# Optimization experiments

Measured on AMD Instinct MI355X. Metric: run time of the kernel, lower is better.

## Reference

```python
import jax, jax.numpy as jnp
import numpy as np

B, N_BOX, NUM_CLASSES = 32, 50, 20
FEATURE_SIZES = np.array([[52, 52], [26, 26], [13, 13]])
NUM_CENG = FEATURE_SIZES[:, 0] * FEATURE_SIZES[:, 1]            # [2704, 676, 169]
NUM_TOTAL = int((NUM_CENG * 3).sum())                            # 10647
ANCS_SCALE = np.array([[10, 13], [16, 30], [33, 23], [30, 61], [62, 45],
                       [59, 119], [116, 90], [156, 198], [373, 326]], dtype=np.float32) / 416.0
NEG_IOU_THRESHOLD = 0.5
NUM_NEG = 1000
EPS = 1e-7

def _build_anchor_grid():
    # rows ordered: level(52,26,13) -> cell (row-major) -> 3 anchors per cell
    out = []
    for lvl in range(3):
        f = int(FEATURE_SIZES[lvl, 0])
        ys, xs = np.meshgrid(np.arange(f), np.arange(f), indexing='ij')
        xy = (np.stack([xs, ys], -1).reshape(-1, 2).astype(np.float32)) / f  # cell corner (col/f,row/f)
        xy3 = np.repeat(xy, 3, axis=0)                                       # [f*f*3, 2]
        wh3 = np.tile(ANCS_SCALE[lvl * 3:(lvl + 1) * 3], (f * f, 1))
        out.append(np.concatenate([xy3, wh3], 1))
    return np.concatenate(out, 0)                                            # [10647, 4]

ANCS = jnp.asarray(_build_anchor_grid())
FSIZES = jnp.asarray(np.repeat(FEATURE_SIZES[:, 0].astype(np.float32), NUM_CENG * 3))  # [10647]
OFF_CENG = jnp.asarray([0.0, 2704.0, 3380.0])   # prefix sums of NUM_CENG
FW_LVL = jnp.asarray([52.0, 26.0, 13.0])


def _xywh2ltrb(xywh):
    return jnp.concatenate([xywh[..., :2] - xywh[..., 2:] * 0.5,
                            xywh[..., :2] + xywh[..., 2:] * 0.5], -1)


def _ciou(a, b):
    # a, b: broadcastable [..., 4] ltrb -> CIoU [...]
    lt = jnp.maximum(a[..., :2], b[..., :2])
    rb = jnp.minimum(a[..., 2:], b[..., 2:])
    wh = jnp.clip(rb - lt, 0.0)
    inter = wh[..., 0] * wh[..., 1]
    wa = a[..., 2] - a[..., 0]; ha = a[..., 3] - a[..., 1]
    wb = b[..., 2] - b[..., 0]; hb = b[..., 3] - b[..., 1]
    union = wa * ha + wb * hb - inter
    iou = inter / (union + EPS)
    clt = jnp.minimum(a[..., :2], b[..., :2])
    crb = jnp.maximum(a[..., 2:], b[..., 2:])
    cwh = crb - clt
    c2 = cwh[..., 0] ** 2 + cwh[..., 1] ** 2 + EPS
    ctr_a = (a[..., :2] + a[..., 2:]) * 0.5
    ctr_b = (b[..., :2] + b[..., 2:]) * 0.5
    rho2 = jnp.sum((ctr_a - ctr_b) ** 2, -1)
    v = (4.0 / (jnp.pi ** 2)) * (jnp.arctan(wa / (ha + EPS)) - jnp.arctan(wb / (hb + EPS))) ** 2
    alpha = jax.lax.stop_gradient(v / (1.0 - iou + v + EPS))
    return iou - rho2 / c2 - alpha * v


def _bce(p, t):
    p = jnp.clip(p, EPS, 1.0 - EPS)
    return -(t * jnp.log(p) + (1.0 - t) * jnp.log(1.0 - p))


def _per_image(p, boxes, labels):
    # p: [10647, 25], boxes: [N,4] ltrb, labels: [N] (1-based)
    N = boxes.shape[0]
    bxy = (boxes[:, :2] + boxes[:, 2:]) * 0.5
    bwh = boxes[:, 2:] - boxes[:, :2]
    # ---- anchor-target matching (source's loop always takes argmax anchor) ----
    p1xy = jnp.repeat(bxy, 9, axis=0)                                       # [N*9, 2]
    fpairs = jnp.repeat(jnp.asarray(FEATURE_SIZES, jnp.float32), 3, axis=0)  # [9, 2]
    p2f = jnp.tile(fpairs, (N, 1))                                          # [N*9, 2]
    colrow = jnp.floor(p1xy * p2f)                                          # (col, row) per box/anchor
    anc_xy = colrow / p2f
    anc_wh = jnp.tile(jnp.asarray(ANCS_SCALE), (N, 1))
    anc_ltrb = _xywh2ltrb(jnp.concatenate([anc_xy, anc_wh], 1))
    ids = jnp.arange(N, dtype=boxes.dtype)
    iou_m = _ciou(boxes[:, None, :] + ids[:, None, None],
                  anc_ltrb[None, :, :] + jnp.repeat(ids, 9)[None, :, None])  # [N, N*9]
    k = jnp.argmax(iou_m, axis=1) % 9                                       # best anchor id 0..8
    lvl = k // 3                                                            # (source quirk: //len(NUMS_ANC))
    cr = colrow[jnp.arange(N) * 9 + k]                                      # [N, 2]
    off_cr = cr[:, 1] * FW_LVL[lvl] + cr[:, 0]
    midx = ((OFF_CENG[lvl] + off_cr) * 3.0 + lvl.astype(jnp.float32)).astype(jnp.int32)  # [N]
    # ---- decode predictions ----
    p_box_xy = p[:, :2] / FSIZES[:, None] + ANCS[:, :2]
    p_box_wh = jnp.exp(p[:, 2:4]) * ANCS[:, 2:]
    p_ltrb = _xywh2ltrb(jnp.concatenate([p_box_xy, p_box_wh], -1))          # [10647, 4]
    # ---- positive losses ----
    pcls = p[midx, 5:]                                                      # [N, C]
    t = jax.nn.one_hot(labels - 1, NUM_CLASSES, dtype=pcls.dtype)
    l_cls = _bce(pcls, t).sum()
    pconf = p[midx, 4]
    l_conf_p = (-jnp.log(jnp.clip(pconf, EPS, 1.0 - EPS))).sum()
    ciou_pos = _ciou(boxes, p_ltrb[midx])                                   # [N]
    w = 2.0 - bwh[:, 0] * bwh[:, 1]
    l_box = (w * (1.0 - ciou_pos)).sum()
    # ---- negative conf loss (replicates filtered-coordinate indexing) ----
    iou_all = _ciou(boxes[:, None, :], p_ltrb[None, :, :])                  # [N, 10647]
    mx = iou_all.max(axis=0)
    mask = mx < NEG_IOU_THRESHOLD
    key = jnp.where(mask, mx, jnp.inf)
    order = jnp.argsort(key)                                                # masked-in first, ascending
    rank = jnp.cumsum(mask) - 1                                             # filtered coordinate per row
    neg_idx = rank[order][:NUM_NEG]                                         # == source's _max_index[:NUM_NEG]
    pneg = p[neg_idx, 4]
    l_conf_n = (-jnp.log(jnp.clip(1.0 - pneg, EPS, 1.0 - EPS))).sum()
    nf = jnp.asarray(N, p.dtype)
    return l_cls / nf, l_box / nf, l_conf_p / nf, l_conf_n


def setup_inputs() -> dict:
    key = jax.random.key(0)
    k1, k2, k3, k4 = jax.random.split(key, 4)
    p_yolo_ts = jax.random.uniform(k1, (B, NUM_TOTAL, 4 + 1 + NUM_CLASSES),
                                   dtype=jnp.float32, minval=1e-4, maxval=1.0 - 1e-4)
    cxy = jax.random.uniform(k2, (B, N_BOX, 2), minval=0.15, maxval=0.85)
    wh = jax.random.uniform(k3, (B, N_BOX, 2), minval=0.05, maxval=0.25)
    boxes = jnp.concatenate([cxy - wh * 0.5, cxy + wh * 0.5], -1).astype(jnp.float32)
    labels = jax.random.randint(k4, (B, N_BOX), 1, NUM_CLASSES + 1, dtype=jnp.int32)
    return {"p_yolo_ts": p_yolo_ts, "boxes": boxes, "labels": labels}


def reference(p_yolo_ts, boxes, labels):
    l_cls, l_box, l_cp, l_cn = jax.vmap(_per_image)(p_yolo_ts, boxes, labels)
    return l_cp.mean() + l_cn.mean() + l_box.mean() + l_cls.mean()
```

## Files before the change

### kernel.cpp

```cpp
#include <hip/hip_runtime.h>

namespace {

constexpr int BB   = 32;
constexpr int NBOX = 50;
constexpr int NCLS = 20;
constexpr int NT   = 10647;
constexpr int NNEG = 1000;
constexpr float EPS = 1e-7f;
constexpr float PI4 = (float)(4.0 / 9.869604401089358);

__device__ __constant__ float c_aw[9] = {10.f/416.f,16.f/416.f,33.f/416.f,30.f/416.f,62.f/416.f,59.f/416.f,116.f/416.f,156.f/416.f,373.f/416.f};
__device__ __constant__ float c_ah[9] = {13.f/416.f,30.f/416.f,23.f/416.f,61.f/416.f,45.f/416.f,119.f/416.f,90.f/416.f,198.f/416.f,326.f/416.f};

__device__ __forceinline__ float fastrcp(float x) {
  return __builtin_amdgcn_rcpf(x);
}

__device__ __forceinline__ float dciou(float al, float at, float ar, float ab,
                                       float bl, float bt, float br, float bb,
                                       float atanA, float atanB) {
  float ltx = fmaxf(al, bl), lty = fmaxf(at, bt);
  float rbx = fminf(ar, br), rby = fminf(ab, bb);
  float wx = fmaxf(rbx - ltx, 0.f), wy = fmaxf(rby - lty, 0.f);
  float inter = wx * wy;
  float wa = ar - al, ha = ab - at;
  float wb = br - bl, hb = bb - bt;
  float uni = wa * ha + wb * hb - inter;
  float iou = inter / (uni + EPS);
  float cw = fmaxf(ar, br) - fminf(al, bl);
  float ch = fmaxf(ab, bb) - fminf(at, bt);
  float c2 = cw * cw + ch * ch + EPS;
  float dx = (al + ar) * 0.5f - (bl + br) * 0.5f;
  float dy = (at + ab) * 0.5f - (bt + bb) * 0.5f;
  float rho2 = dx * dx + dy * dy;
  float dat = atanA - atanB;
  float v = PI4 * (dat * dat);
  float alpha = v / (1.f - iou + v + EPS);
  return iou - rho2 / c2 - alpha * v;
}

__device__ __forceinline__ float dciou_h(float4 A, float4 E,
                                         float bl, float bt, float br, float bb,
                                         float areaB,
                                         float cxb, float cyb, float atanB) {
  float ltx = fmaxf(A.x, bl), lty = fmaxf(A.y, bt);
  float rbx = fminf(A.z, br), rby = fminf(A.w, bb);
  float wx = fmaxf(rbx - ltx, 0.f), wy = fmaxf(rby - lty, 0.f);
  float inter = wx * wy;
  float uni = E.w + areaB - inter;
  float iou = inter * fastrcp(uni + EPS);
  float cw = fmaxf(A.z, br) - fminf(A.x, bl);
  float ch = fmaxf(A.w, bb) - fminf(A.y, bt);
  float c2 = cw * cw + ch * ch + EPS;
  float dx = E.x - cxb;
  float dy = E.y - cyb;
  float rho2 = dx * dx + dy * dy;
  float dat = E.z - atanB;
  float v = PI4 * (dat * dat);
  float alpha = v * fastrcp(1.f - iou + v + EPS);
  return iou - rho2 * fastrcp(c2) - alpha * v;
}

__device__ __forceinline__ int wave_incl_scan(int x, int lane) {
  #pragma unroll
  for (int off = 1; off < 64; off <<= 1) {
    int y = __shfl_up(x, off);
    if (lane >= off) x += y;
  }
  return x;
}

__global__ __launch_bounds__(256) void k_decode_mx(const float* __restrict__ p,
                            const float* __restrict__ boxes,
                            unsigned long long* __restrict__ comp) {
  const int b = blockIdx.y;
  const int tid = threadIdx.x;
  const int par = tid & 1;
  const int j = blockIdx.x * 128 + (tid >> 1);

  __shared__ float4 sA[NBOX];
  __shared__ float4 sE[NBOX];
  if (tid < NBOX) {
    const float* bp = boxes + (b * NBOX + tid) * 4;
    float l = bp[0], t = bp[1], r = bp[2], d = bp[3];
    sA[tid] = make_float4(l, t, r, d);
    float wa = r - l, ha = d - t;
    float cx = (l + r) * 0.5f, cy = (t + d) * 0.5f;
    sE[tid] = make_float4(cx, cy, atanf(wa / (ha + EPS)), wa * ha);
  }
  __syncthreads();
  if (j >= NT) return;

  int lvl, jb0, f;
  if (j < 8112)       { lvl = 0; jb0 = 0;     f = 52; }
  else if (j < 10140) { lvl = 1; jb0 = 8112;  f = 26; }
  else                { lvl = 2; jb0 = 10140; f = 13; }
  int jj = j - jb0;
  int cell = jj / 3, a = jj % 3 + lvl * 3;
  int x = cell % f, y = cell / f;
  float ff = (float)f;
  const float* pr = p + ((size_t)b * NT + j) * 25;
  float px = pr[0] / ff + (float)x / ff;
  float py = pr[1] / ff + (float)y / ff;
  float pw = expf(pr[2]) * c_aw[a];
  float ph = expf(pr[3]) * c_ah[a];
  float bl = px - pw * 0.5f, bt = py - ph * 0.5f;
  float br = px + pw * 0.5f, bbv = py + ph * 0.5f;
  float wb = br - bl, hb = bbv - bt;
  float areab = wb * hb;
  float cxb = (bl + br) * 0.5f, cyb = (bt + bbv) * 0.5f;
  float atb = atanf(wb / (hb + EPS));

  float mx = -INFINITY;
  #pragma unroll 5
  for (int i = par; i < NBOX; i += 2) {
    float v = dciou_h(sA[i], sE[i], bl, bt, br, bbv, areab, cxb, cyb, atb);
    mx = fmaxf(mx, v);
  }
  mx = fmaxf(mx, __shfl_xor(mx, 1));

  if (par == 0) {
    float key = (mx < 0.5f) ? mx : INFINITY;
    unsigned int u = __float_as_uint(key);
    u = (u & 0x80000000u) ? ~u : (u | 0x80000000u);
    comp[(size_t)b * NT + j] = ((unsigned long long)u << 14) | (unsigned long long)j;
  }
}

__global__ __launch_bounds__(1024) void k_neg2(const unsigned long long* __restrict__ comp,
                                               const float* __restrict__ p,
                                               float* __restrict__ lcn) {
  int b = blockIdx.x;
  const unsigned long long* c = comp + (size_t)b * NT;
  const int tid = threadIdx.x, lane = tid & 63, wave = tid >> 6;

  __shared__ int hist[4096];
  __shared__ int s_w[16];
  __shared__ unsigned long long s_pref;
  __shared__ int s_rem;
  __shared__ int s_digit;
  __shared__ int s_rem_next;
  __shared__ int s_cnt;
  __shared__ float s_facc[16];
  __shared__ int s_tot[11][16];
  __shared__ int s_off[11][16];

  unsigned long long v[11];
  #pragma unroll
  for (int k = 0; k < 11; ++k) {
    int j = k * 1024 + tid;
    v[k] = (j < NT) ? c[j] : ~0ull;
  }

  int wincl[11];
  #pragma unroll
  for (int k = 0; k < 11; ++k) {
    unsigned long long x = v[k];
    int flag = ((x >> 14) < 0xFF800000ull) ? 1 : 0;
    int incl = wave_incl_scan(flag, lane);
    wincl[k] = incl;
    if (lane == 63) s_tot[k][wave] = incl;
  }
  __syncthreads();
  if (wave == 0) {
    int i0 = lane * 3;
    int a0 = (i0     < 176) ? s_tot[i0 / 16][i0 % 16] : 0;
    int a1 = (i0 + 1 < 176) ? s_tot[(i0 + 1) / 16][(i0 + 1) % 16] : 0;
    int a2 = (i0 + 2 < 176) ? s_tot[(i0 + 2) / 16][(i0 + 2) % 16] : 0;
    int lsum = a0 + a1 + a2;
    int linc = wave_incl_scan(lsum, lane);
    int lexc = linc - lsum;
    if (i0     < 176) s_off[i0 / 16][i0 % 16] = lexc;
    if (i0 + 1 < 176) s_off[(i0 + 1) / 16][(i0 + 1) % 16] = lexc + a0;
    if (i0 + 2 < 176) s_off[(i0 + 2) / 16][(i0 + 2) % 16] = lexc + a0 + a1;
    if (lane == 63) s_cnt = linc;
  }
  if (tid == 0) { s_pref = 0ull; s_rem = NNEG - 1; }
  __syncthreads();
  const bool spec = (s_cnt >= NNEG);

  for (int pass = 0; pass < 4; ++pass) {
    int lo = 36 - pass * 12;
    for (int h = tid; h < 4096; h += 1024) hist[h] = 0;
    __syncthreads();
    unsigned long long pref = s_pref;
    #pragma unroll
    for (int k = 0; k < 11; ++k) {
      unsigned long long x = v[k];
      bool fin = ((x >> 14) < 0xFF800000ull);
      if ((!spec || fin) && (x >> (lo + 12)) == (pref >> (lo + 12)))
        atomicAdd(&hist[(int)((x >> lo) & 4095ull)], 1);
    }
    __syncthreads();
    int base = tid * 4;
    int c0 = hist[base], c1 = hist[base + 1], c2 = hist[base + 2], c3 = hist[base + 3];
    int tsum = c0 + c1 + c2 + c3;
    int incl = wave_incl_scan(tsum, lane);
    if (lane == 63) s_w[wave] = incl;
    __syncthreads();
    if (wave == 0) {
      int wv = (lane < 16) ? s_w[lane] : 0;
      int wincl2 = wave_incl_scan(wv, lane);
      if (lane < 16) s_w[lane] = wincl2 - wv;
    }
    __syncthreads();
    int excl = incl - tsum + s_w[wave];
    int rem = s_rem;
    int p0 = excl, p1 = p0 + c0, p2 = p1 + c1, p3 = p2 + c2;
    if (rem >= p0 && rem < p0 + c0) { s_digit = base + 0; s_rem_next = rem - p0; }
    if (rem >= p1 && rem < p1 + c1) { s_digit = base + 1; s_rem_next = rem - p1; }
    if (rem >= p2 && rem < p2 + c2) { s_digit = base + 2; s_rem_next = rem - p2; }
    if (rem >= p3 && rem < p3 + c3) { s_digit = base + 3; s_rem_next = rem - p3; }
    __syncthreads();
    if (tid == 0) {
      s_pref |= ((unsigned long long)s_digit) << lo;
      s_rem = s_rem_next;
    }
    __syncthreads();
  }
  const unsigned long long T = s_pref;

  float acc = 0.f;
  const float* pb = p + (size_t)b * NT * 25;
  #pragma unroll
  for (int k = 0; k < 11; ++k) {
    unsigned long long x = v[k];
    if (x <= T) {
      int idx = s_off[k][wave] + wincl[k] - 1;
      if (idx < 0) idx += NT;
      float q = 1.f - pb[(size_t)idx * 25 + 4];
      q = fminf(fmaxf(q, EPS), 1.f - EPS);
      acc += -logf(q);
    }
  }

  #pragma unroll
  for (int off = 32; off > 0; off >>= 1) acc += __shfl_down(acc, off);
  if (lane == 0) s_facc[wave] = acc;
  __syncthreads();
  if (tid == 0) {
    float s = 0.f;
    #pragma unroll
    for (int w = 0; w < 16; ++w) s += s_facc[w];
    lcn[b] = s;
  }
}

__global__ __launch_bounds__(64) void k_pos(const float* __restrict__ p, const float* __restrict__ boxes,
                      const int* __restrict__ labels,
                      float* __restrict__ pcls, float* __restrict__ pbox, float* __restrict__ pcp) {
  const int i = blockIdx.x;
  const int b = blockIdx.y;
  const int lane = threadIdx.x;

  __shared__ float scx[NBOX], scy[NBOX];
  if (lane < NBOX) {
    const float* bp = boxes + (b * NBOX + lane) * 4;
    float l = bp[0], t = bp[1], r = bp[2], d = bp[3];
    scx[lane] = (l + r) * 0.5f;
    scy[lane] = (t + d) * 0.5f;
  }
  __syncthreads();

  const float* bi = boxes + (b * NBOX + i) * 4;
  float bl0 = bi[0], bt0 = bi[1], br0 = bi[2], bd0 = bi[3];
  float fi = (float)i;
  float al = bl0 + fi, at = bt0 + fi, ar = br0 + fi, ad = bd0 + fi;
  float wa = ar - al, ha = ad - at;
  float atanA = atanf(wa / (ha + EPS));

  float bestv = -INFINITY; int bestm = 1 << 30;
  #pragma unroll
  for (int m = lane; m < 9 * NBOX; m += 64) {
    int jb = m / 9, a = m % 9;
    float fa = (a < 3) ? 52.f : (a < 6 ? 26.f : 13.f);
    float col = floorf(scx[jb] * fa);
    float row = floorf(scy[jb] * fa);
    float ax = col / fa, ay = row / fa;
    float aw = c_aw[a], ah = c_ah[a];
    float fj = (float)jb;
    float bl = (ax - aw * 0.5f) + fj;
    float bt = (ay - ah * 0.5f) + fj;
    float br = (ax + aw * 0.5f) + fj;
    float bd = (ay + ah * 0.5f) + fj;
    float wb = br - bl, hb = bd - bt;
    float atanB = atanf(wb / (hb + EPS));
    float v = dciou(al, at, ar, ad, bl, bt, br, bd, atanA, atanB);
    if (v > bestv) { bestv = v; bestm = m; }
  }
  #pragma unroll
  for (int off = 32; off > 0; off >>= 1) {
    float ov = __shfl_down(bestv, off);
    int om = __shfl_down(bestm, off);
    if (ov > bestv || (ov == bestv && om < bestm)) { bestv = ov; bestm = om; }
  }
  int bm = __shfl(bestm, 0);

  int k = bm % 9;
  int lvl = k / 3;
  float fk = (k < 3) ? 52.f : (k < 6 ? 26.f : 13.f);
  float col = floorf(scx[i] * fk);
  float row = floorf(scy[i] * fk);
  float offc = (lvl == 0) ? 0.f : (lvl == 1 ? 2704.f : 3380.f);
  int midx = (int)((offc + row * fk + col) * 3.0f + (float)lvl);

  const float* pr = p + ((size_t)b * NT + midx) * 25;
  int lab = labels[b * NBOX + i] - 1;

  float lc = 0.f;
  if (lane < NCLS) {
    float pc = pr[5 + lane];
    pc = fminf(fmaxf(pc, EPS), 1.f - EPS);
    float tt = (lane == lab) ? 1.f : 0.f;
    lc = -(tt * logf(pc) + (1.f - tt) * logf(1.f - pc));
  }
  #pragma unroll
  for (int off = 32; off > 0; off >>= 1) lc += __shfl_down(lc, off);

  if (lane == 0) {
    pcls[b * NBOX + i] = lc;
    float pc4 = pr[4];
    pc4 = fminf(fmaxf(pc4, EPS), 1.f - EPS);
    pcp[b * NBOX + i] = -logf(pc4);

    int lvl2, jb0, f2;
    if (midx < 8112)       { lvl2 = 0; jb0 = 0;     f2 = 52; }
    else if (midx < 10140) { lvl2 = 1; jb0 = 8112;  f2 = 26; }
    else                   { lvl2 = 2; jb0 = 10140; f2 = 13; }
    int jj2 = midx - jb0;
    int cell2 = jj2 / 3, a2 = jj2 % 3 + lvl2 * 3;
    int xx = cell2 % f2, yy = cell2 / f2;
    float ff2 = (float)f2;
    float px = pr[0] / ff2 + (float)xx / ff2;
    float py = pr[1] / ff2 + (float)yy / ff2;
    float pw = expf(pr[2]) * c_aw[a2];
    float ph = expf(pr[3]) * c_ah[a2];
    float pbl = px - pw * 0.5f, pbt = py - ph * 0.5f;
    float pbr = px + pw * 0.5f, pbd = py + ph * 0.5f;

    float wb = pbr - pbl, hb = pbd - pbt;
    float atanB = atanf(wb / (hb + EPS));
    float wa0 = br0 - bl0, ha0 = bd0 - bt0;
    float atanA0 = atanf(wa0 / (ha0 + EPS));
    float cp = dciou(bl0, bt0, br0, bd0, pbl, pbt, pbr, pbd, atanA0, atanB);
    float w = 2.f - wa0 * ha0;
    pbox[b * NBOX + i] = w * (1.f - cp);
  }
}

__global__ void k_final(const float* __restrict__ pcls, const float* __restrict__ pbox,
                        const float* __restrict__ pcp, const float* __restrict__ lcn,
                        float* __restrict__ out) {
  int lane = threadIdx.x;
  float s = 0.f;
  if (lane < BB) {
    float a = 0.f, bx = 0.f, cp = 0.f;
    for (int i = 0; i < NBOX; ++i) {
      a  += pcls[lane * NBOX + i];
      bx += pbox[lane * NBOX + i];
      cp += pcp[lane * NBOX + i];
    }
    s = (a + bx + cp) / (float)NBOX + lcn[lane];
  }
  #pragma unroll
  for (int off = 32; off > 0; off >>= 1) s += __shfl_down(s, off);
  if (lane == 0) out[0] = s / (float)BB;
}

}

extern "C" void kernel_launch(void* const* d_in, const int* in_sizes, int n_in,
                              void* d_out, int out_size, void* d_ws, size_t ws_size,
                              hipStream_t stream) {
  const float* p      = (const float*)d_in[0];
  const float* boxes  = (const float*)d_in[1];
  const int*   labels = (const int*)d_in[2];
  float* out = (float*)d_out;

  char* ws = (char*)d_ws;
  size_t off = 0;
  unsigned long long* comp = (unsigned long long*)(ws + off); off += (size_t)BB * NT * sizeof(unsigned long long);
  float* pcls = (float*)(ws + off);                off += BB * NBOX * sizeof(float);
  float* pbox = (float*)(ws + off);                off += BB * NBOX * sizeof(float);
  float* pcp  = (float*)(ws + off);                off += BB * NBOX * sizeof(float);
  float* lcn  = (float*)(ws + off);                off += BB * sizeof(float);

  dim3 g1((NT + 127) / 128, BB);
  k_decode_mx<<<g1, 256, 0, stream>>>(p, boxes, comp);
  k_neg2<<<BB, 1024, 0, stream>>>(comp, p, lcn);
  k_pos<<<dim3(NBOX, BB), 64, 0, stream>>>(p, boxes, labels, pcls, pbox, pcp);
  k_final<<<1, 64, 0, stream>>>(pcls, pbox, pcp, lcn, out);
}
```

Baseline: 60.43 us.

## Precompute GT box features in prep kernel and use one thread per anchor

Adds a small k_prep kernel that writes the 8 derived floats per ground-truth box (ltrb, center, atan of aspect, area) to workspace. The decode kernel then reads them as uniform 32-byte vector loads from global memory instead of staging them in shared memory behind a barrier. It also switches from two threads per anchor plus a shuffle to one thread per anchor over all 50 boxes, with index clamping instead of an early return. This removes the per-block atan prologue and the syncthreads, at the cost of an extra kernel launch, half as many blocks and longer serial loops per thread.

```diff
diff --git a/kernel.cpp b/kernel.cpp
--- a/kernel.cpp
+++ b/kernel.cpp
@@ -9,6 +9,8 @@
 constexpr int NNEG = 1000;
 constexpr float EPS = 1e-7f;
 constexpr float PI4 = (float)(4.0 / 9.869604401089358);
+
+typedef __attribute__((ext_vector_type(8))) float f32x8;
 
 __device__ __constant__ float c_aw[9] = {10.f/416.f,16.f/416.f,33.f/416.f,30.f/416.f,62.f/416.f,59.f/416.f,116.f/416.f,156.f/416.f,373.f/416.f};
 __device__ __constant__ float c_ah[9] = {13.f/416.f,30.f/416.f,23.f/416.f,61.f/416.f,45.f/416.f,119.f/416.f,90.f/416.f,198.f/416.f,326.f/416.f};
@@ -40,23 +42,23 @@
   return iou - rho2 / c2 - alpha * v;
 }
 
-__device__ __forceinline__ float dciou_h(float4 A, float4 E,
+__device__ __forceinline__ float dciou_e(f32x8 e,
                                          float bl, float bt, float br, float bb,
                                          float areaB,
                                          float cxb, float cyb, float atanB) {
-  float ltx = fmaxf(A.x, bl), lty = fmaxf(A.y, bt);
-  float rbx = fminf(A.z, br), rby = fminf(A.w, bb);
+  float ltx = fmaxf(e[0], bl), lty = fmaxf(e[1], bt);
+  float rbx = fminf(e[2], br), rby = fminf(e[3], bb);
   float wx = fmaxf(rbx - ltx, 0.f), wy = fmaxf(rby - lty, 0.f);
   float inter = wx * wy;
-  float uni = E.w + areaB - inter;
+  float uni = e[7] + areaB - inter;
   float iou = inter * fastrcp(uni + EPS);
-  float cw = fmaxf(A.z, br) - fminf(A.x, bl);
-  float ch = fmaxf(A.w, bb) - fminf(A.y, bt);
+  float cw = fmaxf(e[2], br) - fminf(e[0], bl);
+  float ch = fmaxf(e[3], bb) - fminf(e[1], bt);
   float c2 = cw * cw + ch * ch + EPS;
-  float dx = E.x - cxb;
-  float dy = E.y - cyb;
+  float dx = e[4] - cxb;
+  float dy = e[5] - cyb;
   float rho2 = dx * dx + dy * dy;
-  float dat = E.z - atanB;
+  float dat = e[6] - atanB;
   float v = PI4 * (dat * dat);
   float alpha = v * fastrcp(1.f - iou + v + EPS);
   return iou - rho2 * fastrcp(c2) - alpha * v;
@@ -71,36 +73,36 @@
   return x;
 }
 
+__global__ __launch_bounds__(64) void k_prep(const float* __restrict__ boxes,
+                                             float* __restrict__ e8) {
+  int b = blockIdx.x, t = threadIdx.x;
+  if (t >= NBOX) return;
+  const float* bp = boxes + (b * NBOX + t) * 4;
+  float l = bp[0], tt = bp[1], r = bp[2], d = bp[3];
+  float wa = r - l, ha = d - tt;
+  float* o = e8 + (b * NBOX + t) * 8;
+  o[0] = l; o[1] = tt; o[2] = r; o[3] = d;
+  o[4] = (l + r) * 0.5f;
+  o[5] = (tt + d) * 0.5f;
+  o[6] = atanf(wa / (ha + EPS));
+  o[7] = wa * ha;
+}
+
 __global__ __launch_bounds__(256) void k_decode_mx(const float* __restrict__ p,
-                            const float* __restrict__ boxes,
+                            const float* __restrict__ e8,
                             unsigned long long* __restrict__ comp) {
   const int b = blockIdx.y;
-  const int tid = threadIdx.x;
-  const int par = tid & 1;
-  const int j = blockIdx.x * 128 + (tid >> 1);
-
-  __shared__ float4 sA[NBOX];
-  __shared__ float4 sE[NBOX];
-  if (tid < NBOX) {
-    const float* bp = boxes + (b * NBOX + tid) * 4;
-    float l = bp[0], t = bp[1], r = bp[2], d = bp[3];
-    sA[tid] = make_float4(l, t, r, d);
-    float wa = r - l, ha = d - t;
-    float cx = (l + r) * 0.5f, cy = (t + d) * 0.5f;
-    sE[tid] = make_float4(cx, cy, atanf(wa / (ha + EPS)), wa * ha);
-  }
-  __syncthreads();
-  if (j >= NT) return;
-
-  int lvl, jb0, f;
-  if (j < 8112)       { lvl = 0; jb0 = 0;     f = 52; }
-  else if (j < 10140) { lvl = 1; jb0 = 8112;  f = 26; }
-  else                { lvl = 2; jb0 = 10140; f = 13; }
-  int jj = j - jb0;
+  const int j = blockIdx.x * 256 + threadIdx.x;
+  const int jc = (j < NT) ? j : (NT - 1);
+
+  int lvl = (jc < 8112) ? 0 : ((jc < 10140) ? 1 : 2);
+  int jb0 = (lvl == 0) ? 0 : ((lvl == 1) ? 8112 : 10140);
+  int f   = (lvl == 0) ? 52 : ((lvl == 1) ? 26 : 13);
+  int jj = jc - jb0;
   int cell = jj / 3, a = jj % 3 + lvl * 3;
   int x = cell % f, y = cell / f;
   float ff = (float)f;
-  const float* pr = p + ((size_t)b * NT + j) * 25;
+  const float* pr = p + ((size_t)b * NT + jc) * 25;
   float px = pr[0] / ff + (float)x / ff;
   float py = pr[1] / ff + (float)y / ff;
   float pw = expf(pr[2]) * c_aw[a];
@@ -112,15 +114,15 @@
   float cxb = (bl + br) * 0.5f, cyb = (bt + bbv) * 0.5f;
   float atb = atanf(wb / (hb + EPS));
 
+  const f32x8* eb = (const f32x8*)(e8 + b * NBOX * 8);
   float mx = -INFINITY;
   #pragma unroll 5
-  for (int i = par; i < NBOX; i += 2) {
-    float v = dciou_h(sA[i], sE[i], bl, bt, br, bbv, areab, cxb, cyb, atb);
+  for (int i = 0; i < NBOX; ++i) {
+    float v = dciou_e(eb[i], bl, bt, br, bbv, areab, cxb, cyb, atb);
     mx = fmaxf(mx, v);
   }
-  mx = fmaxf(mx, __shfl_xor(mx, 1));
-
-  if (par == 0) {
+
+  if (j < NT) {
     float key = (mx < 0.5f) ? mx : INFINITY;
     unsigned int u = __float_as_uint(key);
     u = (u & 0x80000000u) ? ~u : (u | 0x80000000u);
@@ -381,13 +383,15 @@
   char* ws = (char*)d_ws;
   size_t off = 0;
   unsigned long long* comp = (unsigned long long*)(ws + off); off += (size_t)BB * NT * sizeof(unsigned long long);
+  float* e8   = (float*)(ws + off);                off += (size_t)BB * NBOX * 8 * sizeof(float);
   float* pcls = (float*)(ws + off);                off += BB * NBOX * sizeof(float);
   float* pbox = (float*)(ws + off);                off += BB * NBOX * sizeof(float);
   float* pcp  = (float*)(ws + off);                off += BB * NBOX * sizeof(float);
   float* lcn  = (float*)(ws + off);                off += BB * sizeof(float);
 
-  dim3 g1((NT + 127) / 128, BB);
-  k_decode_mx<<<g1, 256, 0, stream>>>(p, boxes, comp);
+  k_prep<<<BB, 64, 0, stream>>>(boxes, e8);
+  dim3 g1((NT + 255) / 256, BB);
+  k_decode_mx<<<g1, 256, 0, stream>>>(p, e8, comp);
   k_neg2<<<BB, 1024, 0, stream>>>(comp, p, lcn);
   k_pos<<<dim3(NBOX, BB), 64, 0, stream>>>(p, boxes, labels, pcls, pbox, pcp);
   k_final<<<1, 64, 0, stream>>>(pcls, pbox, pcp, lcn, out);
```

After: 69.29 us. 14.7% more time.

## Merge positive-match kernel into decode kernel and split box loop four ways

Applied to the files above, without the earlier changes.

Folds the per-GT positive-loss computation into the decode/max-IoU kernel as extra blocks along the grid's x dimension, removing one kernel launch. The decode path now uses 4 threads per prediction (64 predictions per block) instead of 2, doubling the number of blocks for more parallelism, and reduces across the 4 lanes with two xor shuffles. The positive path packs 4 GTs per 256-thread block, one per wave. This trades a launch for a heterogeneous kernel, and the extra shuffles and shorter per-thread loops may or may not pay off.

```diff
diff --git a/kernel.cpp b/kernel.cpp
--- a/kernel.cpp
+++ b/kernel.cpp
@@ -7,6 +7,8 @@
 constexpr int NCLS = 20;
 constexpr int NT   = 10647;
 constexpr int NNEG = 1000;
+constexpr int DEC_BLOCKS = (NT + 63) / 64;
+constexpr int POS_BLOCKS = (NBOX + 3) / 4;
 constexpr float EPS = 1e-7f;
 constexpr float PI4 = (float)(4.0 / 9.869604401089358);
 
@@ -71,60 +73,164 @@
   return x;
 }
 
-__global__ __launch_bounds__(256) void k_decode_mx(const float* __restrict__ p,
+__global__ __launch_bounds__(256) void k_main(const float* __restrict__ p,
                             const float* __restrict__ boxes,
-                            unsigned long long* __restrict__ comp) {
+                            const int* __restrict__ labels,
+                            unsigned long long* __restrict__ comp,
+                            float* __restrict__ pcls, float* __restrict__ pbox,
+                            float* __restrict__ pcp) {
   const int b = blockIdx.y;
   const int tid = threadIdx.x;
-  const int par = tid & 1;
-  const int j = blockIdx.x * 128 + (tid >> 1);
-
-  __shared__ float4 sA[NBOX];
-  __shared__ float4 sE[NBOX];
-  if (tid < NBOX) {
-    const float* bp = boxes + (b * NBOX + tid) * 4;
-    float l = bp[0], t = bp[1], r = bp[2], d = bp[3];
-    sA[tid] = make_float4(l, t, r, d);
-    float wa = r - l, ha = d - t;
-    float cx = (l + r) * 0.5f, cy = (t + d) * 0.5f;
-    sE[tid] = make_float4(cx, cy, atanf(wa / (ha + EPS)), wa * ha);
-  }
-  __syncthreads();
-  if (j >= NT) return;
-
-  int lvl, jb0, f;
-  if (j < 8112)       { lvl = 0; jb0 = 0;     f = 52; }
-  else if (j < 10140) { lvl = 1; jb0 = 8112;  f = 26; }
-  else                { lvl = 2; jb0 = 10140; f = 13; }
-  int jj = j - jb0;
-  int cell = jj / 3, a = jj % 3 + lvl * 3;
-  int x = cell % f, y = cell / f;
-  float ff = (float)f;
-  const float* pr = p + ((size_t)b * NT + j) * 25;
-  float px = pr[0] / ff + (float)x / ff;
-  float py = pr[1] / ff + (float)y / ff;
-  float pw = expf(pr[2]) * c_aw[a];
-  float ph = expf(pr[3]) * c_ah[a];
-  float bl = px - pw * 0.5f, bt = py - ph * 0.5f;
-  float br = px + pw * 0.5f, bbv = py + ph * 0.5f;
-  float wb = br - bl, hb = bbv - bt;
-  float areab = wb * hb;
-  float cxb = (bl + br) * 0.5f, cyb = (bt + bbv) * 0.5f;
-  float atb = atanf(wb / (hb + EPS));
-
-  float mx = -INFINITY;
-  #pragma unroll 5
-  for (int i = par; i < NBOX; i += 2) {
-    float v = dciou_h(sA[i], sE[i], bl, bt, br, bbv, areab, cxb, cyb, atb);
-    mx = fmaxf(mx, v);
-  }
-  mx = fmaxf(mx, __shfl_xor(mx, 1));
-
-  if (par == 0) {
-    float key = (mx < 0.5f) ? mx : INFINITY;
-    unsigned int u = __float_as_uint(key);
-    u = (u & 0x80000000u) ? ~u : (u | 0x80000000u);
-    comp[(size_t)b * NT + j] = ((unsigned long long)u << 14) | (unsigned long long)j;
+
+  if (blockIdx.x < DEC_BLOCKS) {
+    __shared__ float4 sA[NBOX];
+    __shared__ float4 sE[NBOX];
+    if (tid < NBOX) {
+      const float* bp = boxes + (b * NBOX + tid) * 4;
+      float l = bp[0], t = bp[1], r = bp[2], d = bp[3];
+      sA[tid] = make_float4(l, t, r, d);
+      float wa = r - l, ha = d - t;
+      sE[tid] = make_float4((l + r) * 0.5f, (t + d) * 0.5f,
+                            atanf(wa / (ha + EPS)), wa * ha);
+    }
+    __syncthreads();
+
+    const int q = tid & 3;
+    const int j = blockIdx.x * 64 + (tid >> 2);
+    if (j >= NT) return;
+
+    int lvl = (j < 8112) ? 0 : ((j < 10140) ? 1 : 2);
+    int jb0 = (lvl == 0) ? 0 : ((lvl == 1) ? 8112 : 10140);
+    int f   = (lvl == 0) ? 52 : ((lvl == 1) ? 26 : 13);
+    int jj = j - jb0;
+    int cell = jj / 3, a = jj % 3 + lvl * 3;
+    int x = cell % f, y = cell / f;
+    float ff = (float)f;
+    const float* pr = p + ((size_t)b * NT + j) * 25;
+    float px = pr[0] / ff + (float)x / ff;
+    float py = pr[1] / ff + (float)y / ff;
+    float pw = expf(pr[2]) * c_aw[a];
+    float ph = expf(pr[3]) * c_ah[a];
+    float bl = px - pw * 0.5f, bt = py - ph * 0.5f;
+    float br = px + pw * 0.5f, bbv = py + ph * 0.5f;
+    float wb = br - bl, hb = bbv - bt;
+    float areab = wb * hb;
+    float cxb = (bl + br) * 0.5f, cyb = (bt + bbv) * 0.5f;
+    float atb = atanf(wb / (hb + EPS));
+
+    float mx = -INFINITY;
+    #pragma unroll 4
+    for (int i = q; i < NBOX; i += 4) {
+      float v = dciou_h(sA[i], sE[i], bl, bt, br, bbv, areab, cxb, cyb, atb);
+      mx = fmaxf(mx, v);
+    }
+    mx = fmaxf(mx, __shfl_xor(mx, 1));
+    mx = fmaxf(mx, __shfl_xor(mx, 2));
+
+    if (q == 0) {
+      float key = (mx < 0.5f) ? mx : INFINITY;
+      unsigned int u = __float_as_uint(key);
+      u = (u & 0x80000000u) ? ~u : (u | 0x80000000u);
+      comp[(size_t)b * NT + j] = ((unsigned long long)u << 14) | (unsigned long long)j;
+    }
+  } else {
+    const int lane = tid & 63;
+    const int wave = tid >> 6;
+    const int i = (blockIdx.x - DEC_BLOCKS) * 4 + wave;
+
+    __shared__ float scx[NBOX], scy[NBOX];
+    if (tid < NBOX) {
+      const float* bp = boxes + (b * NBOX + tid) * 4;
+      float l = bp[0], t = bp[1], r = bp[2], d = bp[3];
+      scx[tid] = (l + r) * 0.5f;
+      scy[tid] = (t + d) * 0.5f;
+    }
+    __syncthreads();
+    if (i >= NBOX) return;
+
+    const float* bi = boxes + (b * NBOX + i) * 4;
+    float bl0 = bi[0], bt0 = bi[1], br0 = bi[2], bd0 = bi[3];
+    float fi = (float)i;
+    float al = bl0 + fi, at = bt0 + fi, ar = br0 + fi, ad = bd0 + fi;
+    float wa = ar - al, ha = ad - at;
+    float atanA = atanf(wa / (ha + EPS));
+
+    float bestv = -INFINITY; int bestm = 1 << 30;
+    #pragma unroll
+    for (int m = lane; m < 9 * NBOX; m += 64) {
+      int jb = m / 9, aa = m % 9;
+      float fa = (aa < 3) ? 52.f : (aa < 6 ? 26.f : 13.f);
+      float col = floorf(scx[jb] * fa);
+      float row = floorf(scy[jb] * fa);
+      float ax = col / fa, ay = row / fa;
+      float aw = c_aw[aa], ah = c_ah[aa];
+      float fj = (float)jb;
+      float bl = (ax - aw * 0.5f) + fj;
+      float bt = (ay - ah * 0.5f) + fj;
+      float br = (ax + aw * 0.5f) + fj;
+      float bd = (ay + ah * 0.5f) + fj;
+      float wb = br - bl, hb = bd - bt;
+      float atanB = atanf(wb / (hb + EPS));
+      float v = dciou(al, at, ar, ad, bl, bt, br, bd, atanA, atanB);
+      if (v > bestv) { bestv = v; bestm = m; }
+    }
+    #pragma unroll
+    for (int off = 32; off > 0; off >>= 1) {
+      float ov = __shfl_down(bestv, off);
+      int om = __shfl_down(bestm, off);
+      if (ov > bestv || (ov == bestv && om < bestm)) { bestv = ov; bestm = om; }
+    }
+    int bm = __shfl(bestm, 0);
+
+    int k = bm % 9;
+    int lvl = k / 3;
+    float fk = (k < 3) ? 52.f : (k < 6 ? 26.f : 13.f);
+    float col = floorf(scx[i] * fk);
+    float row = floorf(scy[i] * fk);
+    float offc = (lvl == 0) ? 0.f : (lvl == 1 ? 2704.f : 3380.f);
+    int midx = (int)((offc + row * fk + col) * 3.0f + (float)lvl);
+
+    const float* prm = p + ((size_t)b * NT + midx) * 25;
+    int lab = labels[b * NBOX + i] - 1;
+
+    float lc = 0.f;
+    if (lane < NCLS) {
+      float pc = prm[5 + lane];
+      pc = fminf(fmaxf(pc, EPS), 1.f - EPS);
+      float tt = (lane == lab) ? 1.f : 0.f;
+      lc = -(tt * logf(pc) + (1.f - tt) * logf(1.f - pc));
+    }
+    #pragma unroll
+    for (int off = 32; off > 0; off >>= 1) lc += __shfl_down(lc, off);
+
+    if (lane == 0) {
+      pcls[b * NBOX + i] = lc;
+      float pc4 = prm[4];
+      pc4 = fminf(fmaxf(pc4, EPS), 1.f - EPS);
+      pcp[b * NBOX + i] = -logf(pc4);
+
+      int lvl2 = (midx < 8112) ? 0 : ((midx < 10140) ? 1 : 2);
+      int jb0 = (lvl2 == 0) ? 0 : ((lvl2 == 1) ? 8112 : 10140);
+      int f2  = (lvl2 == 0) ? 52 : ((lvl2 == 1) ? 26 : 13);
+      int jj2 = midx - jb0;
+      int cell2 = jj2 / 3, a2 = jj2 % 3 + lvl2 * 3;
+      int xx = cell2 % f2, yy = cell2 / f2;
+      float ff2 = (float)f2;
+      float px = prm[0] / ff2 + (float)xx / ff2;
+      float py = prm[1] / ff2 + (float)yy / ff2;
+      float pw = expf(prm[2]) * c_aw[a2];
+      float ph = expf(prm[3]) * c_ah[a2];
+      float pbl = px - pw * 0.5f, pbt = py - ph * 0.5f;
+      float pbr = px + pw * 0.5f, pbd = py + ph * 0.5f;
+
+      float wb = pbr - pbl, hb = pbd - pbt;
+      float atanB = atanf(wb / (hb + EPS));
+      float wa0 = br0 - bl0, ha0 = bd0 - bt0;
+      float atanA0 = atanf(wa0 / (ha0 + EPS));
+      float cp = dciou(bl0, bt0, br0, bd0, pbl, pbt, pbr, pbd, atanA0, atanB);
+      float w = 2.f - wa0 * ha0;
+      pbox[b * NBOX + i] = w * (1.f - cp);
+    }
   }
 }
 
@@ -247,108 +353,6 @@
   }
 }
 
-__global__ __launch_bounds__(64) void k_pos(const float* __restrict__ p, const float* __restrict__ boxes,
-                      const int* __restrict__ labels,
-                      float* __restrict__ pcls, float* __restrict__ pbox, float* __restrict__ pcp) {
-  const int i = blockIdx.x;
-  const int b = blockIdx.y;
-  const int lane = threadIdx.x;
-
-  __shared__ float scx[NBOX], scy[NBOX];
-  if (lane < NBOX) {
-    const float* bp = boxes + (b * NBOX + lane) * 4;
-    float l = bp[0], t = bp[1], r = bp[2], d = bp[3];
-    scx[lane] = (l + r) * 0.5f;
-    scy[lane] = (t + d) * 0.5f;
-  }
-  __syncthreads();
-
-  const float* bi = boxes + (b * NBOX + i) * 4;
-  float bl0 = bi[0], bt0 = bi[1], br0 = bi[2], bd0 = bi[3];
-  float fi = (float)i;
-  float al = bl0 + fi, at = bt0 + fi, ar = br0 + fi, ad = bd0 + fi;
-  float wa = ar - al, ha = ad - at;
-  float atanA = atanf(wa / (ha + EPS));
-
-  float bestv = -INFINITY; int bestm = 1 << 30;
-  #pragma unroll
-  for (int m = lane; m < 9 * NBOX; m += 64) {
-    int jb = m / 9, a = m % 9;
-    float fa = (a < 3) ? 52.f : (a < 6 ? 26.f : 13.f);
-    float col = floorf(scx[jb] * fa);
-    float row = floorf(scy[jb] * fa);
-    float ax = col / fa, ay = row / fa;
-    float aw = c_aw[a], ah = c_ah[a];
-    float fj = (float)jb;
-    float bl = (ax - aw * 0.5f) + fj;
-    float bt = (ay - ah * 0.5f) + fj;
-    float br = (ax + aw * 0.5f) + fj;
-    float bd = (ay + ah * 0.5f) + fj;
-    float wb = br - bl, hb = bd - bt;
-    float atanB = atanf(wb / (hb + EPS));
-    float v = dciou(al, at, ar, ad, bl, bt, br, bd, atanA, atanB);
-    if (v > bestv) { bestv = v; bestm = m; }
-  }
-  #pragma unroll
-  for (int off = 32; off > 0; off >>= 1) {
-    float ov = __shfl_down(bestv, off);
-    int om = __shfl_down(bestm, off);
-    if (ov > bestv || (ov == bestv && om < bestm)) { bestv = ov; bestm = om; }
-  }
-  int bm = __shfl(bestm, 0);
-
-  int k = bm % 9;
-  int lvl = k / 3;
-  float fk = (k < 3) ? 52.f : (k < 6 ? 26.f : 13.f);
-  float col = floorf(scx[i] * fk);
-  float row = floorf(scy[i] * fk);
-  float offc = (lvl == 0) ? 0.f : (lvl == 1 ? 2704.f : 3380.f);
-  int midx = (int)((offc + row * fk + col) * 3.0f + (float)lvl);
-
-  const float* pr = p + ((size_t)b * NT + midx) * 25;
-  int lab = labels[b * NBOX + i] - 1;
-
-  float lc = 0.f;
-  if (lane < NCLS) {
-    float pc = pr[5 + lane];
-    pc = fminf(fmaxf(pc, EPS), 1.f - EPS);
-    float tt = (lane == lab) ? 1.f : 0.f;
-    lc = -(tt * logf(pc) + (1.f - tt) * logf(1.f - pc));
-  }
-  #pragma unroll
-  for (int off = 32; off > 0; off >>= 1) lc += __shfl_down(lc, off);
-
-  if (lane == 0) {
-    pcls[b * NBOX + i] = lc;
-    float pc4 = pr[4];
-    pc4 = fminf(fmaxf(pc4, EPS), 1.f - EPS);
-    pcp[b * NBOX + i] = -logf(pc4);
-
-    int lvl2, jb0, f2;
-    if (midx < 8112)       { lvl2 = 0; jb0 = 0;     f2 = 52; }
-    else if (midx < 10140) { lvl2 = 1; jb0 = 8112;  f2 = 26; }
-    else                   { lvl2 = 2; jb0 = 10140; f2 = 13; }
-    int jj2 = midx - jb0;
-    int cell2 = jj2 / 3, a2 = jj2 % 3 + lvl2 * 3;
-    int xx = cell2 % f2, yy = cell2 / f2;
-    float ff2 = (float)f2;
-    float px = pr[0] / ff2 + (float)xx / ff2;
-    float py = pr[1] / ff2 + (float)yy / ff2;
-    float pw = expf(pr[2]) * c_aw[a2];
-    float ph = expf(pr[3]) * c_ah[a2];
-    float pbl = px - pw * 0.5f, pbt = py - ph * 0.5f;
-    float pbr = px + pw * 0.5f, pbd = py + ph * 0.5f;
-
-    float wb = pbr - pbl, hb = pbd - pbt;
-    float atanB = atanf(wb / (hb + EPS));
-    float wa0 = br0 - bl0, ha0 = bd0 - bt0;
-    float atanA0 = atanf(wa0 / (ha0 + EPS));
-    float cp = dciou(bl0, bt0, br0, bd0, pbl, pbt, pbr, pbd, atanA0, atanB);
-    float w = 2.f - wa0 * ha0;
-    pbox[b * NBOX + i] = w * (1.f - cp);
-  }
-}
-
 __global__ void k_final(const float* __restrict__ pcls, const float* __restrict__ pbox,
                         const float* __restrict__ pcp, const float* __restrict__ lcn,
                         float* __restrict__ out) {
@@ -386,9 +390,8 @@
   float* pcp  = (float*)(ws + off);                off += BB * NBOX * sizeof(float);
   float* lcn  = (float*)(ws + off);                off += BB * sizeof(float);
 
-  dim3 g1((NT + 127) / 128, BB);
-  k_decode_mx<<<g1, 256, 0, stream>>>(p, boxes, comp);
+  dim3 g1(DEC_BLOCKS + POS_BLOCKS, BB);
+  k_main<<<g1, 256, 0, stream>>>(p, boxes, labels, comp, pcls, pbox, pcp);
   k_neg2<<<BB, 1024, 0, stream>>>(comp, p, lcn);
-  k_pos<<<dim3(NBOX, BB), 64, 0, stream>>>(p, boxes, labels, pcls, pbox, pcp);
   k_final<<<1, 64, 0, stream>>>(pcls, pbox, pcp, lcn, out);
 }
```

Result: slower. 63.01 us (+4.3%).
